# Performance work log

Hardware: AMD Instinct MI355X
Metric: run time of the kernel (lower is better)

## Reference

```python
import jax, jax.numpy as jnp
import numpy as np

H = 64  # hidden_size, hard-coded in module


def _lstm_layer(xs, W_ih, W_hh, b_ih, b_hh):
    """Run one LSTM layer over time-major xs [T, B, D_in].
    PyTorch gate order: i, f, g, o. Returns (hs [T,B,H], h_last [B,H])."""
    T, B, _ = xs.shape
    b = b_ih + b_hh
    # Precompute input contribution for all timesteps: [T, B, 4H]
    x_gates = jnp.einsum('tbd,gd->tbg', xs, W_ih) + b

    def step(carry, xg_t):
        h, c = carry
        gates = xg_t + h @ W_hh.T  # [B, 4H]
        i, f, g, o = jnp.split(gates, 4, axis=-1)
        i = jax.nn.sigmoid(i)
        f = jax.nn.sigmoid(f)
        g = jnp.tanh(g)
        o = jax.nn.sigmoid(o)
        c = f * c + i * g
        h = o * jnp.tanh(c)
        return (h, c), h

    h0 = jnp.zeros((B, H), xs.dtype)
    c0 = jnp.zeros((B, H), xs.dtype)
    (h_last, _), hs = jax.lax.scan(step, (h0, c0), x_gates)
    return hs, h_last


def setup_inputs() -> dict:
    key = jax.random.key(0)
    ks = jax.random.split(key, 12)
    B, T, C_in, E = 256, 4000, 1, 128
    s0 = 1.0 / np.sqrt(H)  # PyTorch LSTM init scale
    inp = {
        'x': jax.random.normal(ks[0], (B, T, C_in), jnp.float32),
        'W_ih0': jax.random.uniform(ks[1], (4 * H, C_in), jnp.float32, -s0, s0),
        'W_hh0': jax.random.uniform(ks[2], (4 * H, H), jnp.float32, -s0, s0),
        'b_ih0': jax.random.uniform(ks[3], (4 * H,), jnp.float32, -s0, s0),
        'b_hh0': jax.random.uniform(ks[4], (4 * H,), jnp.float32, -s0, s0),
        'W_ih1': jax.random.uniform(ks[5], (4 * H, H), jnp.float32, -s0, s0),
        'W_hh1': jax.random.uniform(ks[6], (4 * H, H), jnp.float32, -s0, s0),
        'b_ih1': jax.random.uniform(ks[7], (4 * H,), jnp.float32, -s0, s0),
        'b_hh1': jax.random.uniform(ks[8], (4 * H,), jnp.float32, -s0, s0),
        'W_fc': jax.random.uniform(ks[9], (E, H), jnp.float32, -s0, s0),
        'b_fc': jax.random.uniform(ks[10], (E,), jnp.float32, -s0, s0),
    }
    return inp


def reference(x, W_ih0, W_hh0, b_ih0, b_hh0, W_ih1, W_hh1, b_ih1, b_hh1, W_fc, b_fc):
    # x: [B, T, 1] (batch_first) -> time-major [T, B, 1]
    xs = jnp.swapaxes(x.astype(jnp.float32), 0, 1)
    hs0, _ = _lstm_layer(xs, W_ih0, W_hh0, b_ih0, b_hh0)
    _, h_last = _lstm_layer(hs0, W_ih1, W_hh1, b_ih1, b_hh1)
    # fc on final hidden state of the last layer: [B, E]
    return h_last @ W_fc.T + b_fc
```

## Files before the change

kernel.cpp:

```cpp
#include <hip/hip_runtime.h>

#define TT 4000
#define HH 64
#define NB 256
#define EE 128

typedef __attribute__((ext_vector_type(8))) _Float16 h8;
typedef __attribute__((ext_vector_type(4))) float f4;

__device__ __forceinline__ float ftanh(float x) {
    return fmaf(2.f, __builtin_amdgcn_rcpf(1.f + __expf(-2.f * x)), -1.f);
}
__device__ __forceinline__ float fsig(float x) {
    return __builtin_amdgcn_rcpf(1.f + __expf(-x));
}

#define MF(A, B, C) __builtin_amdgcn_mfma_f32_16x16x32_f16((A), (B), (C), 0, 0, 0)

__device__ __forceinline__ h8 ld8h(const float* p) {
    f4 a = ((const f4*)p)[0], c = ((const f4*)p)[1];
    return h8{(_Float16)a.x, (_Float16)a.y, (_Float16)a.z, (_Float16)a.w,
              (_Float16)c.x, (_Float16)c.y, (_Float16)c.z, (_Float16)c.w};
}

__global__ __launch_bounds__(256, 1)
void lstm2_fc_kernel(const float* __restrict__ x,
                     const float* __restrict__ W_ih0,
                     const float* __restrict__ W_hh0,
                     const float* __restrict__ b_ih0,
                     const float* __restrict__ b_hh0,
                     const float* __restrict__ W_ih1,
                     const float* __restrict__ W_hh1,
                     const float* __restrict__ b_ih1,
                     const float* __restrict__ b_hh1,
                     const float* __restrict__ W_fc,
                     const float* __restrict__ b_fc,
                     float* __restrict__ out)
{
    const int b    = blockIdx.x;
    const int tid  = threadIdx.x;
    const int w    = tid >> 6;
    const int lane = tid & 63;
    const int cidx = lane & 15;
    const int kgrp = lane >> 4;
    const int n    = w * 16 + cidx;
    const bool act = (kgrp == 0);

    __shared__ float x_s[TT];
    __shared__ __align__(16) _Float16 hbuf[2][2 * HH];

    for (int t = tid; t < TT; t += 256) x_s[t] = x[(size_t)b * TT + t];
    if (tid < 4 * HH) ((_Float16*)hbuf)[tid] = (_Float16)0.f;

    const int rI = 0 * HH + n, rF = 1 * HH + n, rG = 2 * HH + n, rO = 3 * HH + n;
    const int kb0 = kgrp * 8, kb1 = 32 + kgrp * 8;

    h8 BI0a = ld8h(W_hh0 + rI * HH + kb0), BI0b = ld8h(W_hh0 + rI * HH + kb1);
    h8 BF0a = ld8h(W_hh0 + rF * HH + kb0), BF0b = ld8h(W_hh0 + rF * HH + kb1);
    h8 BG0a = ld8h(W_hh0 + rG * HH + kb0), BG0b = ld8h(W_hh0 + rG * HH + kb1);
    h8 BO0a = ld8h(W_hh0 + rO * HH + kb0), BO0b = ld8h(W_hh0 + rO * HH + kb1);
    h8 BI1a = ld8h(W_ih1 + rI * HH + kb0), BI1b = ld8h(W_ih1 + rI * HH + kb1);
    h8 BF1a = ld8h(W_ih1 + rF * HH + kb0), BF1b = ld8h(W_ih1 + rF * HH + kb1);
    h8 BG1a = ld8h(W_ih1 + rG * HH + kb0), BG1b = ld8h(W_ih1 + rG * HH + kb1);
    h8 BO1a = ld8h(W_ih1 + rO * HH + kb0), BO1b = ld8h(W_ih1 + rO * HH + kb1);
    h8 BI1c = ld8h(W_hh1 + rI * HH + kb0), BI1d = ld8h(W_hh1 + rI * HH + kb1);
    h8 BF1c = ld8h(W_hh1 + rF * HH + kb0), BF1d = ld8h(W_hh1 + rF * HH + kb1);
    h8 BG1c = ld8h(W_hh1 + rG * HH + kb0), BG1d = ld8h(W_hh1 + rG * HH + kb1);
    h8 BO1c = ld8h(W_hh1 + rO * HH + kb0), BO1d = ld8h(W_hh1 + rO * HH + kb1);

    float wxI = W_ih0[rI], wxF = W_ih0[rF], wxG = W_ih0[rG], wxO = W_ih0[rO];
    float bI0 = b_ih0[rI] + b_hh0[rI], bF0 = b_ih0[rF] + b_hh0[rF];
    float bG0 = b_ih0[rG] + b_hh0[rG], bO0 = b_ih0[rO] + b_hh0[rO];
    float bI1 = b_ih1[rI] + b_hh1[rI], bF1 = b_ih1[rF] + b_hh1[rF];
    float bG1 = b_ih1[rG] + b_hh1[rG], bO1 = b_ih1[rO] + b_hh1[rO];

    asm volatile("" : "+v"(BI0a), "+v"(BI0b), "+v"(BF0a), "+v"(BF0b),
                      "+v"(BG0a), "+v"(BG0b), "+v"(BO0a), "+v"(BO0b),
                      "+v"(BI1a), "+v"(BI1b), "+v"(BF1a), "+v"(BF1b));
    asm volatile("" : "+v"(BG1a), "+v"(BG1b), "+v"(BO1a), "+v"(BO1b),
                      "+v"(BI1c), "+v"(BI1d), "+v"(BF1c), "+v"(BF1d),
                      "+v"(BG1c), "+v"(BG1d), "+v"(BO1c), "+v"(BO1d));
    asm volatile("" : "+v"(wxI), "+v"(wxF), "+v"(wxG), "+v"(wxO),
                      "+v"(bI0), "+v"(bF0), "+v"(bG0), "+v"(bO0),
                      "+v"(bI1), "+v"(bF1), "+v"(bG1), "+v"(bO1));

    float cc0 = 0.f, cc1 = 0.f;

    __syncthreads();

    for (int t = 0; t <= TT; ++t) {
        const float xt = x_s[(t < TT) ? t : 0];
        const h8* hb = (const h8*)hbuf[t & 1];
        h8 A0a = hb[kgrp],     A0b = hb[4 + kgrp];
        h8 A1a = hb[8 + kgrp], A1b = hb[12 + kgrp];

        f4 aI0 = {act ? fmaf(xt, wxI, bI0) : 0.f, 0.f, 0.f, 0.f};
        f4 aF0 = {act ? fmaf(xt, wxF, bF0) : 0.f, 0.f, 0.f, 0.f};
        f4 aG0 = {act ? fmaf(xt, wxG, bG0) : 0.f, 0.f, 0.f, 0.f};
        f4 aO0 = {act ? fmaf(xt, wxO, bO0) : 0.f, 0.f, 0.f, 0.f};
        f4 aI1 = {act ? bI1 : 0.f, 0.f, 0.f, 0.f};
        f4 aF1 = {act ? bF1 : 0.f, 0.f, 0.f, 0.f};
        f4 aG1 = {act ? bG1 : 0.f, 0.f, 0.f, 0.f};
        f4 aO1 = {act ? bO1 : 0.f, 0.f, 0.f, 0.f};

        aI0 = MF(A0a, BI0a, aI0); aF0 = MF(A0a, BF0a, aF0);
        aG0 = MF(A0a, BG0a, aG0); aO0 = MF(A0a, BO0a, aO0);
        aI0 = MF(A0b, BI0b, aI0); aF0 = MF(A0b, BF0b, aF0);
        aG0 = MF(A0b, BG0b, aG0); aO0 = MF(A0b, BO0b, aO0);
        aI1 = MF(A0a, BI1a, aI1); aF1 = MF(A0a, BF1a, aF1);
        aG1 = MF(A0a, BG1a, aG1); aO1 = MF(A0a, BO1a, aO1);
        aI1 = MF(A0b, BI1b, aI1); aF1 = MF(A0b, BF1b, aF1);
        aG1 = MF(A0b, BG1b, aG1); aO1 = MF(A0b, BO1b, aO1);
        aI1 = MF(A1a, BI1c, aI1); aF1 = MF(A1a, BF1c, aF1);
        aG1 = MF(A1a, BG1c, aG1); aO1 = MF(A1a, BO1c, aO1);
        aI1 = MF(A1b, BI1d, aI1); aF1 = MF(A1b, BF1d, aF1);
        aG1 = MF(A1b, BG1d, aG1); aO1 = MF(A1b, BO1d, aO1);

        float i0 = fsig(aI0.x), f0v = fsig(aF0.x);
        float g0 = ftanh(aG0.x), o0 = fsig(aO0.x);
        float i1 = fsig(aI1.x), f1v = fsig(aF1.x);
        float g1 = ftanh(aG1.x), o1 = fsig(aO1.x);
        float nc0 = fmaf(f0v, cc0, i0 * g0);
        float nc1 = fmaf(f1v, cc1, i1 * g1);
        const bool ok0 = (t < TT), ok1 = (t > 0);
        cc0 = ok0 ? nc0 : cc0;
        cc1 = ok1 ? nc1 : cc1;
        float h0n = o0 * ftanh(nc0);
        float h1n = o1 * ftanh(nc1);
        _Float16* hw = hbuf[(t + 1) & 1];
        if (act && ok0) hw[n] = (_Float16)h0n;
        if (act && ok1) hw[HH + n] = (_Float16)h1n;

        __syncthreads();
    }

    if (tid < EE) {
        const _Float16* h1f = &hbuf[(TT + 1) & 1][HH];
        float acc = b_fc[tid];
        const float4* wf = (const float4*)(W_fc + tid * HH);
        #pragma unroll
        for (int k = 0; k < HH / 4; ++k) {
            float4 v = wf[k];
            acc = fmaf(v.x, (float)h1f[4*k+0], acc);
            acc = fmaf(v.y, (float)h1f[4*k+1], acc);
            acc = fmaf(v.z, (float)h1f[4*k+2], acc);
            acc = fmaf(v.w, (float)h1f[4*k+3], acc);
        }
        out[(size_t)b * EE + tid] = acc;
    }
}

extern "C" void kernel_launch(void* const* d_in, const int* in_sizes, int n_in,
                              void* d_out, int out_size, void* d_ws, size_t ws_size,
                              hipStream_t stream) {
    const float* x     = (const float*)d_in[0];
    const float* W_ih0 = (const float*)d_in[1];
    const float* W_hh0 = (const float*)d_in[2];
    const float* b_ih0 = (const float*)d_in[3];
    const float* b_hh0 = (const float*)d_in[4];
    const float* W_ih1 = (const float*)d_in[5];
    const float* W_hh1 = (const float*)d_in[6];
    const float* b_ih1 = (const float*)d_in[7];
    const float* b_hh1 = (const float*)d_in[8];
    const float* W_fc  = (const float*)d_in[9];
    const float* b_fc  = (const float*)d_in[10];
    float* out = (float*)d_out;

    lstm2_fc_kernel<<<dim3(NB), dim3(256), 0, stream>>>(
        x, W_ih0, W_hh0, b_ih0, b_hh0, W_ih1, W_hh1, b_ih1, b_hh1, W_fc, b_fc, out);
}
```

Before: 2.082 ms.

## Compute layer-0 recurrence via per-lane fdot2 and spread gate activations across lanes

Layer 0's recurrent matvec moves off MFMA. Each lane now owns one gate row and computes its 64-wide dot product with packed fp16 fdot2 instructions. Gate nonlinearities are spread so each of the four lane groups evaluates one gate type, and ds_bpermute gathers the i, f, g, o values per hidden unit. Layer-0 and layer-1 state writes are split between kgrp 0 and kgrp 1 lanes. The aim is to shorten the per-timestep serial chain by removing half the MFMA chain and the redundant activation work on idle lanes, at the cost of a long dependent fdot2 chain, eight LDS broadcast reads and extra cross-lane permutes.

Result: slower. 2.231 ms (+7.2%).

```diff
diff --git a/kernel.cpp b/kernel.cpp
--- a/kernel.cpp
+++ b/kernel.cpp
@@ -5,17 +5,26 @@
 #define NB 256
 #define EE 128
 
+typedef __attribute__((ext_vector_type(2))) _Float16 h2;
 typedef __attribute__((ext_vector_type(8))) _Float16 h8;
 typedef __attribute__((ext_vector_type(4))) float f4;
 
 __device__ __forceinline__ float ftanh(float x) {
     return fmaf(2.f, __builtin_amdgcn_rcpf(1.f + __expf(-2.f * x)), -1.f);
 }
-__device__ __forceinline__ float fsig(float x) {
-    return __builtin_amdgcn_rcpf(1.f + __expf(-x));
-}
-
+
+#if __has_builtin(__builtin_amdgcn_fdot2)
+#define FDOT2(a, b, c) __builtin_amdgcn_fdot2((a), (b), (c), false)
+#else
+#define FDOT2(a, b, c) fmaf((float)(a).x, (float)(b).x, fmaf((float)(a).y, (float)(b).y, (c)))
+#endif
+
+#define H2V(V, i) (__builtin_shufflevector((V), (V), 2 * (i), 2 * (i) + 1))
 #define MF(A, B, C) __builtin_amdgcn_mfma_f32_16x16x32_f16((A), (B), (C), 0, 0, 0)
+
+__device__ __forceinline__ float bperm(int addr, float v) {
+    return __int_as_float(__builtin_amdgcn_ds_bpermute(addr, __float_as_int(v)));
+}
 
 __device__ __forceinline__ h8 ld8h(const float* p) {
     f4 a = ((const f4*)p)[0], c = ((const f4*)p)[1];
@@ -41,10 +50,9 @@
     const int tid  = threadIdx.x;
     const int w    = tid >> 6;
     const int lane = tid & 63;
-    const int cidx = lane & 15;
+    const int c    = lane & 15;
     const int kgrp = lane >> 4;
-    const int n    = w * 16 + cidx;
-    const bool act = (kgrp == 0);
+    const int n    = w * 16 + c;
 
     __shared__ float x_s[TT];
     __shared__ __align__(16) _Float16 hbuf[2][2 * HH];
@@ -52,13 +60,15 @@
     for (int t = tid; t < TT; t += 256) x_s[t] = x[(size_t)b * TT + t];
     if (tid < 4 * HH) ((_Float16*)hbuf)[tid] = (_Float16)0.f;
 
+    const int rL = kgrp * HH + n;
     const int rI = 0 * HH + n, rF = 1 * HH + n, rG = 2 * HH + n, rO = 3 * HH + n;
     const int kb0 = kgrp * 8, kb1 = 32 + kgrp * 8;
 
-    h8 BI0a = ld8h(W_hh0 + rI * HH + kb0), BI0b = ld8h(W_hh0 + rI * HH + kb1);
-    h8 BF0a = ld8h(W_hh0 + rF * HH + kb0), BF0b = ld8h(W_hh0 + rF * HH + kb1);
-    h8 BG0a = ld8h(W_hh0 + rG * HH + kb0), BG0b = ld8h(W_hh0 + rG * HH + kb1);
-    h8 BO0a = ld8h(W_hh0 + rO * HH + kb0), BO0b = ld8h(W_hh0 + rO * HH + kb1);
+    h8 Wl0 = ld8h(W_hh0 + rL * HH + 0),  Wl1 = ld8h(W_hh0 + rL * HH + 8);
+    h8 Wl2 = ld8h(W_hh0 + rL * HH + 16), Wl3 = ld8h(W_hh0 + rL * HH + 24);
+    h8 Wl4 = ld8h(W_hh0 + rL * HH + 32), Wl5 = ld8h(W_hh0 + rL * HH + 40);
+    h8 Wl6 = ld8h(W_hh0 + rL * HH + 48), Wl7 = ld8h(W_hh0 + rL * HH + 56);
+
     h8 BI1a = ld8h(W_ih1 + rI * HH + kb0), BI1b = ld8h(W_ih1 + rI * HH + kb1);
     h8 BF1a = ld8h(W_ih1 + rF * HH + kb0), BF1b = ld8h(W_ih1 + rF * HH + kb1);
     h8 BG1a = ld8h(W_ih1 + rG * HH + kb0), BG1b = ld8h(W_ih1 + rG * HH + kb1);
@@ -68,23 +78,31 @@
     h8 BG1c = ld8h(W_hh1 + rG * HH + kb0), BG1d = ld8h(W_hh1 + rG * HH + kb1);
     h8 BO1c = ld8h(W_hh1 + rO * HH + kb0), BO1d = ld8h(W_hh1 + rO * HH + kb1);
 
-    float wxI = W_ih0[rI], wxF = W_ih0[rF], wxG = W_ih0[rG], wxO = W_ih0[rO];
-    float bI0 = b_ih0[rI] + b_hh0[rI], bF0 = b_ih0[rF] + b_hh0[rF];
-    float bG0 = b_ih0[rG] + b_hh0[rG], bO0 = b_ih0[rO] + b_hh0[rO];
+    float wx  = W_ih0[rL];
+    float bb0 = b_ih0[rL] + b_hh0[rL];
     float bI1 = b_ih1[rI] + b_hh1[rI], bF1 = b_ih1[rF] + b_hh1[rF];
     float bG1 = b_ih1[rG] + b_hh1[rG], bO1 = b_ih1[rO] + b_hh1[rO];
 
-    asm volatile("" : "+v"(BI0a), "+v"(BI0b), "+v"(BF0a), "+v"(BF0b),
-                      "+v"(BG0a), "+v"(BG0b), "+v"(BO0a), "+v"(BO0b),
+    asm volatile("" : "+v"(Wl0), "+v"(Wl1), "+v"(Wl2), "+v"(Wl3),
+                      "+v"(Wl4), "+v"(Wl5), "+v"(Wl6), "+v"(Wl7),
                       "+v"(BI1a), "+v"(BI1b), "+v"(BF1a), "+v"(BF1b));
     asm volatile("" : "+v"(BG1a), "+v"(BG1b), "+v"(BO1a), "+v"(BO1b),
                       "+v"(BI1c), "+v"(BI1d), "+v"(BF1c), "+v"(BF1d),
                       "+v"(BG1c), "+v"(BG1d), "+v"(BO1c), "+v"(BO1d));
-    asm volatile("" : "+v"(wxI), "+v"(wxF), "+v"(wxG), "+v"(wxO),
-                      "+v"(bI0), "+v"(bF0), "+v"(bG0), "+v"(bO0),
+    asm volatile("" : "+v"(wx), "+v"(bb0),
                       "+v"(bI1), "+v"(bF1), "+v"(bG1), "+v"(bO1));
 
+    const bool isg = (kgrp == 2);
+    const float kk = isg ? -2.f : -1.f;
+    const float mm = isg ?  2.f :  1.f;
+    const float aa = isg ? -1.f :  0.f;
+
+    const int ai = 4 * (0 * 16 + c), af = 4 * (1 * 16 + c);
+    const int ag = 4 * (2 * 16 + c), ao = 4 * (3 * 16 + c);
+
     float cc0 = 0.f, cc1 = 0.f;
+    f4 aI1 = {0.f, 0.f, 0.f, 0.f}, aF1 = {0.f, 0.f, 0.f, 0.f};
+    f4 aG1 = {0.f, 0.f, 0.f, 0.f}, aO1 = {0.f, 0.f, 0.f, 0.f};
 
     __syncthreads();
 
@@ -93,20 +111,10 @@
         const h8* hb = (const h8*)hbuf[t & 1];
         h8 A0a = hb[kgrp],     A0b = hb[4 + kgrp];
         h8 A1a = hb[8 + kgrp], A1b = hb[12 + kgrp];
-
-        f4 aI0 = {act ? fmaf(xt, wxI, bI0) : 0.f, 0.f, 0.f, 0.f};
-        f4 aF0 = {act ? fmaf(xt, wxF, bF0) : 0.f, 0.f, 0.f, 0.f};
-        f4 aG0 = {act ? fmaf(xt, wxG, bG0) : 0.f, 0.f, 0.f, 0.f};
-        f4 aO0 = {act ? fmaf(xt, wxO, bO0) : 0.f, 0.f, 0.f, 0.f};
-        f4 aI1 = {act ? bI1 : 0.f, 0.f, 0.f, 0.f};
-        f4 aF1 = {act ? bF1 : 0.f, 0.f, 0.f, 0.f};
-        f4 aG1 = {act ? bG1 : 0.f, 0.f, 0.f, 0.f};
-        f4 aO1 = {act ? bO1 : 0.f, 0.f, 0.f, 0.f};
-
-        aI0 = MF(A0a, BI0a, aI0); aF0 = MF(A0a, BF0a, aF0);
-        aG0 = MF(A0a, BG0a, aG0); aO0 = MF(A0a, BO0a, aO0);
-        aI0 = MF(A0b, BI0b, aI0); aF0 = MF(A0b, BF0b, aF0);
-        aG0 = MF(A0b, BG0b, aG0); aO0 = MF(A0b, BO0b, aO0);
+        h8 H0 = hb[0], H1 = hb[1], H2 = hb[2], H3 = hb[3];
+        h8 H4 = hb[4], H5 = hb[5], H6 = hb[6], H7 = hb[7];
+
+        aI1.x = bI1; aF1.x = bF1; aG1.x = bG1; aO1.x = bO1;
         aI1 = MF(A0a, BI1a, aI1); aF1 = MF(A0a, BF1a, aF1);
         aG1 = MF(A0a, BG1a, aG1); aO1 = MF(A0a, BO1a, aO1);
         aI1 = MF(A0b, BI1b, aI1); aF1 = MF(A0b, BF1b, aF1);
@@ -116,20 +124,46 @@
         aI1 = MF(A1b, BI1d, aI1); aF1 = MF(A1b, BF1d, aF1);
         aG1 = MF(A1b, BG1d, aG1); aO1 = MF(A1b, BO1d, aO1);
 
-        float i0 = fsig(aI0.x), f0v = fsig(aF0.x);
-        float g0 = ftanh(aG0.x), o0 = fsig(aO0.x);
-        float i1 = fsig(aI1.x), f1v = fsig(aF1.x);
-        float g1 = ftanh(aG1.x), o1 = fsig(aO1.x);
-        float nc0 = fmaf(f0v, cc0, i0 * g0);
-        float nc1 = fmaf(f1v, cc1, i1 * g1);
+        float z0 = fmaf(xt, wx, bb0);
+        z0 = FDOT2(H2V(Wl0,0), H2V(H0,0), z0); z0 = FDOT2(H2V(Wl0,1), H2V(H0,1), z0);
+        z0 = FDOT2(H2V(Wl0,2), H2V(H0,2), z0); z0 = FDOT2(H2V(Wl0,3), H2V(H0,3), z0);
+        z0 = FDOT2(H2V(Wl1,0), H2V(H1,0), z0); z0 = FDOT2(H2V(Wl1,1), H2V(H1,1), z0);
+        z0 = FDOT2(H2V(Wl1,2), H2V(H1,2), z0); z0 = FDOT2(H2V(Wl1,3), H2V(H1,3), z0);
+        z0 = FDOT2(H2V(Wl2,0), H2V(H2,0), z0); z0 = FDOT2(H2V(Wl2,1), H2V(H2,1), z0);
+        z0 = FDOT2(H2V(Wl2,2), H2V(H2,2), z0); z0 = FDOT2(H2V(Wl2,3), H2V(H2,3), z0);
+        z0 = FDOT2(H2V(Wl3,0), H2V(H3,0), z0); z0 = FDOT2(H2V(Wl3,1), H2V(H3,1), z0);
+        z0 = FDOT2(H2V(Wl3,2), H2V(H3,2), z0); z0 = FDOT2(H2V(Wl3,3), H2V(H3,3), z0);
+        z0 = FDOT2(H2V(Wl4,0), H2V(H4,0), z0); z0 = FDOT2(H2V(Wl4,1), H2V(H4,1), z0);
+        z0 = FDOT2(H2V(Wl4,2), H2V(H4,2), z0); z0 = FDOT2(H2V(Wl4,3), H2V(H4,3), z0);
+        z0 = FDOT2(H2V(Wl5,0), H2V(H5,0), z0); z0 = FDOT2(H2V(Wl5,1), H2V(H5,1), z0);
+        z0 = FDOT2(H2V(Wl5,2), H2V(H5,2), z0); z0 = FDOT2(H2V(Wl5,3), H2V(H5,3), z0);
+        z0 = FDOT2(H2V(Wl6,0), H2V(H6,0), z0); z0 = FDOT2(H2V(Wl6,1), H2V(H6,1), z0);
+        z0 = FDOT2(H2V(Wl6,2), H2V(H6,2), z0); z0 = FDOT2(H2V(Wl6,3), H2V(H6,3), z0);
+        z0 = FDOT2(H2V(Wl7,0), H2V(H7,0), z0); z0 = FDOT2(H2V(Wl7,1), H2V(H7,1), z0);
+        z0 = FDOT2(H2V(Wl7,2), H2V(H7,2), z0); z0 = FDOT2(H2V(Wl7,3), H2V(H7,3), z0);
+
+        float e0  = __expf(kk * z0);
+        float av0 = fmaf(mm, __builtin_amdgcn_rcpf(1.f + e0), aa);
+        float i0 = bperm(ai, av0), f0 = bperm(af, av0);
+        float g0 = bperm(ag, av0), o0 = bperm(ao, av0);
+        float cn0 = fmaf(f0, cc0, i0 * g0);
         const bool ok0 = (t < TT), ok1 = (t > 0);
-        cc0 = ok0 ? nc0 : cc0;
-        cc1 = ok1 ? nc1 : cc1;
-        float h0n = o0 * ftanh(nc0);
-        float h1n = o1 * ftanh(nc1);
+        cc0 = ok0 ? cn0 : cc0;
+        float h0n = o0 * ftanh(cn0);
+
+        float z1 = (kgrp & 2) ? ((kgrp & 1) ? aO1.x : aG1.x)
+                              : ((kgrp & 1) ? aF1.x : aI1.x);
+        float e1  = __expf(kk * z1);
+        float av1 = fmaf(mm, __builtin_amdgcn_rcpf(1.f + e1), aa);
+        float i1 = bperm(ai, av1), f1 = bperm(af, av1);
+        float g1 = bperm(ag, av1), o1 = bperm(ao, av1);
+        float cn1 = fmaf(f1, cc1, i1 * g1);
+        cc1 = ok1 ? cn1 : cc1;
+        float h1n = o1 * ftanh(cn1);
+
         _Float16* hw = hbuf[(t + 1) & 1];
-        if (act && ok0) hw[n] = (_Float16)h0n;
-        if (act && ok1) hw[HH + n] = (_Float16)h1n;
+        if (kgrp == 0 && ok0) hw[n] = (_Float16)h0n;
+        if (kgrp == 1 && ok1) hw[HH + n] = (_Float16)h1n;
 
         __syncthreads();
     }
```
